# Performance work log

Measured on AMD Instinct MI355X. Metric: run time of the kernel, lower is better.

## Reference

```python
import jax, jax.numpy as jnp
import numpy as np

N = 200000          # nodes
E = 6400000         # edges (avg degree 32)
IN_C, HID, OUT_C = 128, 16, 2


def gcn_conv(x, W, b, src, dst, n):
    """PyG GCNConv: out = D^{-1/2} (A + I) D^{-1/2} (x W) + b."""
    h = x @ W  # transform first (in_channels >= out_channels): [n, d_out]
    loop = jnp.arange(n)
    s = jnp.concatenate([src, loop])  # add self-loops
    d = jnp.concatenate([dst, loop])
    ew = jnp.ones(s.shape[0], x.dtype)
    deg = jax.ops.segment_sum(ew, d, num_segments=n)  # in-degree incl. self-loop
    dinv = jnp.where(deg > 0, jax.lax.rsqrt(deg), jnp.zeros((), x.dtype))
    norm = dinv[s] * dinv[d]                          # [E+n]
    msg = h[s] * norm[:, None]                        # gather + scale
    out = jax.ops.segment_sum(msg, d, num_segments=n) # scatter-add
    return out + b


def setup_inputs() -> dict:
    key = jax.random.key(0)
    k1, k2, k3, k4 = jax.random.split(key, 4)
    x = jax.random.normal(k1, (N, IN_C), dtype=jnp.float32)
    edge_index = jax.random.randint(k2, (2, E), 0, N, dtype=jnp.int64)
    # Glorot-style init like PyG GCNConv
    W1 = jax.random.normal(k3, (IN_C, HID), dtype=jnp.float32) * (1.0 / np.sqrt(IN_C))
    b1 = jnp.zeros((HID,), jnp.float32)
    W2 = jax.random.normal(k4, (HID, OUT_C), dtype=jnp.float32) * (1.0 / np.sqrt(HID))
    b2 = jnp.zeros((OUT_C,), jnp.float32)
    return {"x": x, "edge_index": edge_index, "W1": W1, "b1": b1, "W2": W2, "b2": b2}


def reference(x, edge_index, W1, b1, W2, b2):
    src, dst = edge_index[0], edge_index[1]
    h = gcn_conv(x, W1, b1, src, dst, N)
    h = jax.nn.relu(h)
    return gcn_conv(h, W2, b2, src, dst, N)
```

## Files before the change

### kernel.cpp

```cpp
#include <hip/hip_runtime.h>
#include <hip/hip_fp16.h>

#define NN   200000
#define EE   6400000
#define INC  128
#define HIDC 16
#define OUTC 2

#define TN     256
#define TSHIFT 8
#define TMASK  (TN - 1)
#define NT     782
#define CHUNK  8192
#define NBE    782
#define SCAP   10240

__global__ __launch_bounds__(256) void k_hist(const int* __restrict__ dst,
                                              int* __restrict__ tile_counts) {
    __shared__ int h[NT];
    for (int t = threadIdx.x; t < NT; t += 256) h[t] = 0;
    __syncthreads();
    int base = blockIdx.x * CHUNK;
    if (base + CHUNK <= EE) {
        for (int i = threadIdx.x; i < CHUNK; i += 1024) {
            int d0 = dst[base + i];
            int d1 = dst[base + i + 256];
            int d2 = dst[base + i + 512];
            int d3 = dst[base + i + 768];
            atomicAdd(&h[d0 >> TSHIFT], 1);
            atomicAdd(&h[d1 >> TSHIFT], 1);
            atomicAdd(&h[d2 >> TSHIFT], 1);
            atomicAdd(&h[d3 >> TSHIFT], 1);
        }
    } else {
        for (int i = threadIdx.x; i < CHUNK; i += 256) {
            int e = base + i;
            if (e < EE) atomicAdd(&h[dst[e] >> TSHIFT], 1);
        }
    }
    __syncthreads();
    for (int t = threadIdx.x; t < NT; t += 256) {
        int c = h[t];
        if (c) atomicAdd(&tile_counts[t], c);
    }
}

__global__ __launch_bounds__(1024) void k_scan(const int* __restrict__ tile_counts,
                                               int* __restrict__ tile_base,
                                               int* __restrict__ gcur) {
    __shared__ int tmp[1024];
    int t = threadIdx.x;
    int v = (t < NT) ? tile_counts[t] : 0;
    tmp[t] = v;
    __syncthreads();
    for (int o = 1; o < 1024; o <<= 1) {
        int u = (t >= o) ? tmp[t - o] : 0;
        __syncthreads();
        tmp[t] += u;
        __syncthreads();
    }
    if (t < NT) {
        int ex = tmp[t] - v;
        tile_base[t] = ex;
        gcur[t] = ex;
    }
}

__global__ __launch_bounds__(256) void k_place(const int* __restrict__ src,
                                               const int* __restrict__ dst,
                                               int* __restrict__ gcur,
                                               int* __restrict__ brec) {
    __shared__ int h[NT];
    __shared__ int lbase[NT];
    __shared__ int gofs[NT];
    __shared__ int stmp[256];
    __shared__ int lrec[CHUNK];
    __shared__ unsigned short ltid[CHUNK];

    int tid = threadIdx.x;
    int base = blockIdx.x * CHUNK;
    int nrec = EE - base; if (nrec > CHUNK) nrec = CHUNK;
    bool full = (base + CHUNK <= EE);

    for (int t = tid; t < NT; t += 256) h[t] = 0;
    __syncthreads();
    if (full) {
        for (int i = tid; i < CHUNK; i += 1024) {
            int d0 = dst[base + i];
            int d1 = dst[base + i + 256];
            int d2 = dst[base + i + 512];
            int d3 = dst[base + i + 768];
            atomicAdd(&h[d0 >> TSHIFT], 1);
            atomicAdd(&h[d1 >> TSHIFT], 1);
            atomicAdd(&h[d2 >> TSHIFT], 1);
            atomicAdd(&h[d3 >> TSHIFT], 1);
        }
    } else {
        for (int i = tid; i < nrec; i += 256)
            atomicAdd(&h[dst[base + i] >> TSHIFT], 1);
    }
    __syncthreads();

    int t0 = tid * 4;
    int c0 = (t0 + 0 < NT) ? h[t0 + 0] : 0;
    int c1 = (t0 + 1 < NT) ? h[t0 + 1] : 0;
    int c2 = (t0 + 2 < NT) ? h[t0 + 2] : 0;
    int c3 = (t0 + 3 < NT) ? h[t0 + 3] : 0;
    int s = c0 + c1 + c2 + c3;
    stmp[tid] = s;
    __syncthreads();
    for (int o = 1; o < 256; o <<= 1) {
        int u = (tid >= o) ? stmp[tid - o] : 0;
        __syncthreads();
        stmp[tid] += u;
        __syncthreads();
    }
    int run = stmp[tid] - s;
    if (t0 + 0 < NT) { lbase[t0 + 0] = run; run += c0; }
    if (t0 + 1 < NT) { lbase[t0 + 1] = run; run += c1; }
    if (t0 + 2 < NT) { lbase[t0 + 2] = run; run += c2; }
    if (t0 + 3 < NT) { lbase[t0 + 3] = run; run += c3; }
    __syncthreads();

    for (int t = tid; t < NT; t += 256) {
        int c = h[t];
        int gb = c ? atomicAdd(&gcur[t], c) : 0;
        gofs[t] = gb - lbase[t];
    }
    __syncthreads();

    if (full) {
        for (int i = tid; i < CHUNK; i += 1024) {
            int e = base + i;
            int d0 = dst[e], d1 = dst[e + 256], d2 = dst[e + 512], d3 = dst[e + 768];
            int s0 = src[e], s1 = src[e + 256], s2 = src[e + 512], s3 = src[e + 768];
            int t0_ = d0 >> TSHIFT, t1_ = d1 >> TSHIFT;
            int t2_ = d2 >> TSHIFT, t3_ = d3 >> TSHIFT;
            int p0 = atomicAdd(&lbase[t0_], 1);
            int p1 = atomicAdd(&lbase[t1_], 1);
            int p2 = atomicAdd(&lbase[t2_], 1);
            int p3 = atomicAdd(&lbase[t3_], 1);
            lrec[p0] = (s0 << 8) | (d0 & TMASK); ltid[p0] = (unsigned short)t0_;
            lrec[p1] = (s1 << 8) | (d1 & TMASK); ltid[p1] = (unsigned short)t1_;
            lrec[p2] = (s2 << 8) | (d2 & TMASK); ltid[p2] = (unsigned short)t2_;
            lrec[p3] = (s3 << 8) | (d3 & TMASK); ltid[p3] = (unsigned short)t3_;
        }
    } else {
        for (int i = tid; i < nrec; i += 256) {
            int e = base + i;
            int d = dst[e], ss = src[e];
            int tt = d >> TSHIFT;
            int p = atomicAdd(&lbase[tt], 1);
            lrec[p] = (ss << 8) | (d & TMASK); ltid[p] = (unsigned short)tt;
        }
    }
    __syncthreads();

    for (int i = tid; i < nrec; i += 256) {
        int r = lrec[i];
        int tt = ltid[i];
        brec[gofs[tt] + i] = r;
    }
}

__global__ __launch_bounds__(256) void k_sortt(int* __restrict__ brec,
                                               const int* __restrict__ tile_base,
                                               const int* __restrict__ tile_counts,
                                               int* __restrict__ nstart,
                                               int* __restrict__ ndeg) {
    __shared__ int rec[SCAP];
    __shared__ int hist[TN];
    __shared__ int scn[TN];
    __shared__ int cur[TN];
    int t = blockIdx.x;
    int s0 = tile_base[t];
    int cnt = tile_counts[t];
    if (cnt > SCAP) cnt = SCAP;
    if (threadIdx.x < TN) hist[threadIdx.x] = 0;
    __syncthreads();
    for (int i = threadIdx.x; i < cnt; i += 256) {
        int r = brec[s0 + i];
        rec[i] = r;
        atomicAdd(&hist[r & TMASK], 1);
    }
    __syncthreads();
    if (threadIdx.x < TN) scn[threadIdx.x] = hist[threadIdx.x];
    __syncthreads();
    for (int o = 1; o < TN; o <<= 1) {
        int u = (threadIdx.x >= o && threadIdx.x < TN) ? scn[threadIdx.x - o] : 0;
        __syncthreads();
        if (threadIdx.x < TN) scn[threadIdx.x] += u;
        __syncthreads();
    }
    if (threadIdx.x < TN) {
        int ex = scn[threadIdx.x] - hist[threadIdx.x];
        cur[threadIdx.x] = ex;
        int node = t * TN + threadIdx.x;
        if (node < NN) {
            nstart[node] = s0 + ex;
            ndeg[node] = hist[threadIdx.x];
        }
    }
    __syncthreads();
    for (int i = threadIdx.x; i < cnt; i += 256) {
        int r = rec[i];
        int pos = atomicAdd(&cur[r & TMASK], 1);
        brec[s0 + pos] = r >> 8;
    }
}

__global__ __launch_bounds__(256) void k_xw(const float* __restrict__ x,
                                            const float* __restrict__ W1,
                                            const int* __restrict__ ndeg,
                                            __half2* __restrict__ g1) {
    __shared__ float Ws[INC * HIDC];
    for (int j = threadIdx.x; j < INC * HIDC; j += 256) Ws[j] = W1[j];
    __syncthreads();
    int n = blockIdx.x * 256 + threadIdx.x;
    if (n >= NN) return;
    const float4* xr = (const float4*)(x + (size_t)n * INC);
    float acc[HIDC];
#pragma unroll
    for (int c = 0; c < HIDC; ++c) acc[c] = 0.f;
    for (int k4 = 0; k4 < INC / 4; ++k4) {
        float4 xv = xr[k4];
        const float* w0 = &Ws[(k4 * 4) * HIDC];
        float xs[4] = {xv.x, xv.y, xv.z, xv.w};
#pragma unroll
        for (int j = 0; j < 4; ++j) {
#pragma unroll
            for (int c = 0; c < HIDC; ++c) acc[c] += xs[j] * w0[j * HIDC + c];
        }
    }
    float dn = rsqrtf((float)(ndeg[n] + 1));
    union { __half2 h[8]; float4 f[2]; } u;
#pragma unroll
    for (int q = 0; q < 8; ++q)
        u.h[q] = __floats2half2_rn(dn * acc[2 * q], dn * acc[2 * q + 1]);
    float4* gp = (float4*)(g1 + (size_t)n * 8);
    gp[0] = u.f[0];
    gp[1] = u.f[1];
}

__global__ __launch_bounds__(256) void k_agg1n(const int* __restrict__ csr,
                                               const int* __restrict__ nstart,
                                               const int* __restrict__ ndeg,
                                               const __half2* __restrict__ g1,
                                               const float* __restrict__ b1,
                                               const float* __restrict__ W2,
                                               float* __restrict__ g2) {
    int lane = threadIdx.x & 7;
    int n = (blockIdx.x * 256 + threadIdx.x) >> 3;
    if (n >= NN) return;
    int rs = nstart[n];
    int deg = ndeg[n];
    int re = rs + deg;
    float dn = rsqrtf((float)(deg + 1));
    float2 s = __half22float2(g1[(size_t)n * 8 + lane]);
    float ax = s.x, ay = s.y;
    int i = rs;
    for (; i + 4 <= re; i += 4) {
        int s0 = csr[i], s1 = csr[i + 1], s2 = csr[i + 2], s3 = csr[i + 3];
        float2 f0 = __half22float2(g1[(size_t)s0 * 8 + lane]);
        float2 f1 = __half22float2(g1[(size_t)s1 * 8 + lane]);
        float2 f2 = __half22float2(g1[(size_t)s2 * 8 + lane]);
        float2 f3 = __half22float2(g1[(size_t)s3 * 8 + lane]);
        ax += f0.x + f1.x + f2.x + f3.x;
        ay += f0.y + f1.y + f2.y + f3.y;
    }
    for (; i < re; ++i) {
        float2 f = __half22float2(g1[(size_t)csr[i] * 8 + lane]);
        ax += f.x; ay += f.y;
    }
    float h0 = fmaxf(fmaf(dn, ax, b1[2 * lane]), 0.f);
    float h1 = fmaxf(fmaf(dn, ay, b1[2 * lane + 1]), 0.f);
    float p0 = h0 * W2[(2 * lane) * OUTC + 0] + h1 * W2[(2 * lane + 1) * OUTC + 0];
    float p1 = h0 * W2[(2 * lane) * OUTC + 1] + h1 * W2[(2 * lane + 1) * OUTC + 1];
#pragma unroll
    for (int o = 4; o; o >>= 1) {
        p0 += __shfl_xor(p0, o, 8);
        p1 += __shfl_xor(p1, o, 8);
    }
    if (lane == 0) {
        float2 v; v.x = dn * p0; v.y = dn * p1;
        ((float2*)g2)[n] = v;
    }
}

__global__ __launch_bounds__(256) void k_agg2n(const int* __restrict__ csr,
                                               const int* __restrict__ nstart,
                                               const int* __restrict__ ndeg,
                                               const float* __restrict__ g2,
                                               const float* __restrict__ b2,
                                               float* __restrict__ out) {
    int lane = threadIdx.x & 7;
    int n = (blockIdx.x * 256 + threadIdx.x) >> 3;
    if (n >= NN) return;
    int rs = nstart[n];
    int deg = ndeg[n];
    int re = rs + deg;
    float dn = rsqrtf((float)(deg + 1));
    float ax = 0.f, ay = 0.f;
    for (int i = rs + lane; i < re; i += 8) {
        float2 v = ((const float2*)g2)[csr[i]];
        ax += v.x; ay += v.y;
    }
#pragma unroll
    for (int o = 4; o; o >>= 1) {
        ax += __shfl_xor(ax, o, 8);
        ay += __shfl_xor(ay, o, 8);
    }
    if (lane == 0) {
        float2 g = ((const float2*)g2)[n];
        float2 o2;
        o2.x = fmaf(dn, ax + g.x, b2[0]);
        o2.y = fmaf(dn, ay + g.y, b2[1]);
        ((float2*)out)[n] = o2;
    }
}


__global__ void k_deg_f(const int* __restrict__ dst, int* __restrict__ deg) {
    int i = blockIdx.x * blockDim.x + threadIdx.x;
    if (i < EE) atomicAdd(&deg[dst[i]], 1);
}
__global__ void k_dinv_f(const int* __restrict__ deg, float* __restrict__ dinv) {
    int n = blockIdx.x * blockDim.x + threadIdx.x;
    if (n < NN) dinv[n] = rsqrtf((float)(deg[n] + 1));
}
__global__ void k_xw_f(const float* __restrict__ x, const float* __restrict__ W1,
                       const float* __restrict__ dinv, float* __restrict__ g1) {
    __shared__ float Ws[INC * HIDC];
    for (int j = threadIdx.x; j < INC * HIDC; j += 256) Ws[j] = W1[j];
    __syncthreads();
    int n = blockIdx.x * 256 + threadIdx.x;
    if (n >= NN) return;
    const float4* xr = (const float4*)(x + (size_t)n * INC);
    float acc[HIDC];
#pragma unroll
    for (int c = 0; c < HIDC; ++c) acc[c] = 0.f;
    for (int k4 = 0; k4 < INC / 4; ++k4) {
        float4 xv = xr[k4];
        const float* w0 = &Ws[(k4 * 4) * HIDC];
        float xs[4] = {xv.x, xv.y, xv.z, xv.w};
#pragma unroll
        for (int j = 0; j < 4; ++j)
#pragma unroll
            for (int c = 0; c < HIDC; ++c) acc[c] += xs[j] * w0[j * HIDC + c];
    }
    float dn = dinv[n];
#pragma unroll
    for (int c = 0; c < HIDC; ++c) g1[(size_t)n * HIDC + c] = dn * acc[c];
}
__global__ void k_scatter1_f(const int* __restrict__ src, const int* __restrict__ dst,
                             const float* __restrict__ g1, float* __restrict__ acc1) {
    int i = blockIdx.x * blockDim.x + threadIdx.x;
    if (i >= EE * 4) return;
    int e = i >> 2, q = i & 3;
    float4 v = ((const float4*)g1)[src[e] * 4 + q];
    float* p = acc1 + (size_t)dst[e] * HIDC + q * 4;
    unsafeAtomicAdd(p + 0, v.x); unsafeAtomicAdd(p + 1, v.y);
    unsafeAtomicAdd(p + 2, v.z); unsafeAtomicAdd(p + 3, v.w);
}
__global__ void k_l2_f(const float* __restrict__ g1, const float* __restrict__ acc1,
                       const float* __restrict__ dinv, const float* __restrict__ b1,
                       const float* __restrict__ W2, float* __restrict__ g2) {
    int n = blockIdx.x * blockDim.x + threadIdx.x;
    if (n >= NN) return;
    float dn = dinv[n];
    float h[HIDC];
#pragma unroll
    for (int c = 0; c < HIDC; ++c)
        h[c] = fmaxf(dn * (acc1[(size_t)n * HIDC + c] + g1[(size_t)n * HIDC + c]) + b1[c], 0.f);
    float o0 = 0.f, o1 = 0.f;
#pragma unroll
    for (int c = 0; c < HIDC; ++c) { o0 += h[c] * W2[c * 2]; o1 += h[c] * W2[c * 2 + 1]; }
    g2[(size_t)n * 2] = dn * o0; g2[(size_t)n * 2 + 1] = dn * o1;
}
__global__ void k_scatter2_f(const int* __restrict__ src, const int* __restrict__ dst,
                             const float* __restrict__ g2, float* __restrict__ acc2) {
    int e = blockIdx.x * blockDim.x + threadIdx.x;
    if (e >= EE) return;
    float2 v = ((const float2*)g2)[src[e]];
    unsafeAtomicAdd(&acc2[(size_t)dst[e] * 2], v.x);
    unsafeAtomicAdd(&acc2[(size_t)dst[e] * 2 + 1], v.y);
}
__global__ void k_final_f(const float* __restrict__ g2, const float* __restrict__ acc2,
                          const float* __restrict__ dinv, const float* __restrict__ b2,
                          float* __restrict__ out) {
    int n = blockIdx.x * blockDim.x + threadIdx.x;
    if (n >= NN) return;
    float dn = dinv[n];
    float2 a = ((const float2*)acc2)[n];
    float2 g = ((const float2*)g2)[n];
    float2 o;
    o.x = dn * (a.x + g.x) + b2[0];
    o.y = dn * (a.y + g.y) + b2[1];
    ((float2*)out)[n] = o;
}


extern "C" void kernel_launch(void* const* d_in, const int* in_sizes, int n_in,
                              void* d_out, int out_size, void* d_ws, size_t ws_size,
                              hipStream_t stream) {
    const float* x  = (const float*)d_in[0];
    const int*   ei = (const int*)d_in[1];
    const float* W1 = (const float*)d_in[2];
    const float* b1 = (const float*)d_in[3];
    const float* W2 = (const float*)d_in[4];
    const float* b2 = (const float*)d_in[5];
    float* out = (float*)d_out;

    const int* src = ei;
    const int* dst = ei + EE;
    const int B = 256;

    size_t need = ((size_t)3 * NT + EE + (size_t)(NN + 1) + (size_t)NN +
                   (size_t)8 * NN + (size_t)2 * NN) * 4;
    if (ws_size >= need) {
        int* ws          = (int*)d_ws;
        int* tile_counts = ws;
        int* tile_base   = ws + NT;
        int* gcur        = ws + 2 * NT;
        int* brec        = ws + 3 * NT;
        int* nstart      = brec + EE;
        int* ndeg        = nstart + NN + 1;
        __half2* g1      = (__half2*)(ndeg + NN);
        float* g2        = (float*)((int*)(ndeg + NN) + (size_t)8 * NN);

        hipMemsetAsync(tile_counts, 0, (size_t)NT * 4, stream);

        k_hist  <<<NBE, 256, 0, stream>>>(dst, tile_counts);
        k_scan  <<<1, 1024, 0, stream>>>(tile_counts, tile_base, gcur);
        k_place <<<NBE, 256, 0, stream>>>(src, dst, gcur, brec);
        k_sortt <<<NT, 256, 0, stream>>>(brec, tile_base, tile_counts, nstart, ndeg);
        k_xw    <<<(NN + 255) / 256, 256, 0, stream>>>(x, W1, ndeg, g1);
        k_agg1n <<<(NN * 8 + 255) / 256, 256, 0, stream>>>(brec, nstart, ndeg, g1, b1, W2, g2);
        k_agg2n <<<(NN * 8 + 255) / 256, 256, 0, stream>>>(brec, nstart, ndeg, g2, b2, out);
        return;
    }

    char* wsb = (char*)d_ws;
    int*   deg  = (int*)wsb;
    float* acc1 = (float*)(wsb + (size_t)NN * 4);
    float* acc2 = (float*)(wsb + (size_t)17 * NN * 4);
    float* dinv = (float*)(wsb + (size_t)19 * NN * 4);
    float* g1   = (float*)(wsb + (size_t)20 * NN * 4);
    float* g2   = (float*)(wsb + (size_t)36 * NN * 4);

    hipMemsetAsync(d_ws, 0, (size_t)19 * NN * 4, stream);

    int gN = (NN + B - 1) / B, gE = (EE + B - 1) / B, gE4 = (EE * 4 + B - 1) / B;
    k_deg_f     <<<gE, B, 0, stream>>>(dst, deg);
    k_dinv_f    <<<gN, B, 0, stream>>>(deg, dinv);
    k_xw_f      <<<gN, B, 0, stream>>>(x, W1, dinv, g1);
    k_scatter1_f<<<gE4, B, 0, stream>>>(src, dst, g1, acc1);
    k_l2_f      <<<gN, B, 0, stream>>>(g1, acc1, dinv, b1, W2, g2);
    k_scatter2_f<<<gE, B, 0, stream>>>(src, dst, g2, acc2);
    k_final_f   <<<gN, B, 0, stream>>>(g2, acc2, dinv, b2, out);
}
```

Before: 451.0 us.

## Split layer-1 feature table into two halves and aggregate in two passes

The fp16 hidden-feature table is split into two 8-channel halves of 3.2 MB each, written separately by the XW kernel. Layer-1 aggregation runs as two passes, each gathering from one half with 4 lanes per node, so the random-access working set is smaller and more likely to stay in cache. In exchange the CSR index array and node metadata are read twice, and a partial-result buffer is written and then read back between the passes.

Measured after the change: 474.8 us. +5.3%, slower.

```diff
diff --git a/kernel.cpp b/kernel.cpp
--- a/kernel.cpp
+++ b/kernel.cpp
@@ -212,7 +212,8 @@
 __global__ __launch_bounds__(256) void k_xw(const float* __restrict__ x,
                                             const float* __restrict__ W1,
                                             const int* __restrict__ ndeg,
-                                            __half2* __restrict__ g1) {
+                                            __half2* __restrict__ g1a,
+                                            __half2* __restrict__ g1b) {
     __shared__ float Ws[INC * HIDC];
     for (int j = threadIdx.x; j < INC * HIDC; j += 256) Ws[j] = W1[j];
     __syncthreads();
@@ -237,53 +238,58 @@
 #pragma unroll
     for (int q = 0; q < 8; ++q)
         u.h[q] = __floats2half2_rn(dn * acc[2 * q], dn * acc[2 * q + 1]);
-    float4* gp = (float4*)(g1 + (size_t)n * 8);
-    gp[0] = u.f[0];
-    gp[1] = u.f[1];
-}
-
-__global__ __launch_bounds__(256) void k_agg1n(const int* __restrict__ csr,
+    ((float4*)(g1a + (size_t)n * 4))[0] = u.f[0];
+    ((float4*)(g1b + (size_t)n * 4))[0] = u.f[1];
+}
+
+__global__ __launch_bounds__(256) void k_agg1h(const int* __restrict__ csr,
                                                const int* __restrict__ nstart,
                                                const int* __restrict__ ndeg,
-                                               const __half2* __restrict__ g1,
+                                               const __half2* __restrict__ tab,
                                                const float* __restrict__ b1,
                                                const float* __restrict__ W2,
-                                               float* __restrict__ g2) {
-    int lane = threadIdx.x & 7;
-    int n = (blockIdx.x * 256 + threadIdx.x) >> 3;
+                                               float* __restrict__ pacc,
+                                               float* __restrict__ g2,
+                                               int cofs, int phase) {
+    int lane = threadIdx.x & 3;
+    int n = (blockIdx.x * 256 + threadIdx.x) >> 2;
     if (n >= NN) return;
     int rs = nstart[n];
     int deg = ndeg[n];
     int re = rs + deg;
     float dn = rsqrtf((float)(deg + 1));
-    float2 s = __half22float2(g1[(size_t)n * 8 + lane]);
-    float ax = s.x, ay = s.y;
+    float2 sl = __half22float2(tab[(size_t)n * 4 + lane]);
+    float ax = sl.x, ay = sl.y;
     int i = rs;
     for (; i + 4 <= re; i += 4) {
         int s0 = csr[i], s1 = csr[i + 1], s2 = csr[i + 2], s3 = csr[i + 3];
-        float2 f0 = __half22float2(g1[(size_t)s0 * 8 + lane]);
-        float2 f1 = __half22float2(g1[(size_t)s1 * 8 + lane]);
-        float2 f2 = __half22float2(g1[(size_t)s2 * 8 + lane]);
-        float2 f3 = __half22float2(g1[(size_t)s3 * 8 + lane]);
+        float2 f0 = __half22float2(tab[(size_t)s0 * 4 + lane]);
+        float2 f1 = __half22float2(tab[(size_t)s1 * 4 + lane]);
+        float2 f2 = __half22float2(tab[(size_t)s2 * 4 + lane]);
+        float2 f3 = __half22float2(tab[(size_t)s3 * 4 + lane]);
         ax += f0.x + f1.x + f2.x + f3.x;
         ay += f0.y + f1.y + f2.y + f3.y;
     }
     for (; i < re; ++i) {
-        float2 f = __half22float2(g1[(size_t)csr[i] * 8 + lane]);
+        float2 f = __half22float2(tab[(size_t)csr[i] * 4 + lane]);
         ax += f.x; ay += f.y;
     }
-    float h0 = fmaxf(fmaf(dn, ax, b1[2 * lane]), 0.f);
-    float h1 = fmaxf(fmaf(dn, ay, b1[2 * lane + 1]), 0.f);
-    float p0 = h0 * W2[(2 * lane) * OUTC + 0] + h1 * W2[(2 * lane + 1) * OUTC + 0];
-    float p1 = h0 * W2[(2 * lane) * OUTC + 1] + h1 * W2[(2 * lane + 1) * OUTC + 1];
-#pragma unroll
-    for (int o = 4; o; o >>= 1) {
-        p0 += __shfl_xor(p0, o, 8);
-        p1 += __shfl_xor(p1, o, 8);
-    }
+    int c0 = cofs + 2 * lane;
+    float h0 = fmaxf(fmaf(dn, ax, b1[c0]), 0.f);
+    float h1 = fmaxf(fmaf(dn, ay, b1[c0 + 1]), 0.f);
+    float p0 = h0 * W2[c0 * OUTC + 0] + h1 * W2[(c0 + 1) * OUTC + 0];
+    float p1 = h0 * W2[c0 * OUTC + 1] + h1 * W2[(c0 + 1) * OUTC + 1];
+    p0 += __shfl_xor(p0, 1, 4); p0 += __shfl_xor(p0, 2, 4);
+    p1 += __shfl_xor(p1, 1, 4); p1 += __shfl_xor(p1, 2, 4);
     if (lane == 0) {
-        float2 v; v.x = dn * p0; v.y = dn * p1;
-        ((float2*)g2)[n] = v;
+        if (phase == 0) {
+            float2 v; v.x = p0; v.y = p1;
+            ((float2*)pacc)[n] = v;
+        } else {
+            float2 pa = ((const float2*)pacc)[n];
+            float2 v; v.x = dn * (p0 + pa.x); v.y = dn * (p1 + pa.y);
+            ((float2*)g2)[n] = v;
+        }
     }
 }
 
@@ -416,7 +422,7 @@
     const int B = 256;
 
     size_t need = ((size_t)3 * NT + EE + (size_t)(NN + 1) + (size_t)NN +
-                   (size_t)8 * NN + (size_t)2 * NN) * 4;
+                   (size_t)4 * NN + (size_t)4 * NN + (size_t)2 * NN + (size_t)2 * NN) * 4;
     if (ws_size >= need) {
         int* ws          = (int*)d_ws;
         int* tile_counts = ws;
@@ -425,8 +431,10 @@
         int* brec        = ws + 3 * NT;
         int* nstart      = brec + EE;
         int* ndeg        = nstart + NN + 1;
-        __half2* g1      = (__half2*)(ndeg + NN);
-        float* g2        = (float*)((int*)(ndeg + NN) + (size_t)8 * NN);
+        __half2* g1a     = (__half2*)(ndeg + NN);
+        __half2* g1b     = g1a + (size_t)4 * NN;
+        float* pacc      = (float*)(g1b + (size_t)4 * NN);
+        float* g2        = pacc + (size_t)2 * NN;
 
         hipMemsetAsync(tile_counts, 0, (size_t)NT * 4, stream);
 
@@ -434,8 +442,9 @@
         k_scan  <<<1, 1024, 0, stream>>>(tile_counts, tile_base, gcur);
         k_place <<<NBE, 256, 0, stream>>>(src, dst, gcur, brec);
         k_sortt <<<NT, 256, 0, stream>>>(brec, tile_base, tile_counts, nstart, ndeg);
-        k_xw    <<<(NN + 255) / 256, 256, 0, stream>>>(x, W1, ndeg, g1);
-        k_agg1n <<<(NN * 8 + 255) / 256, 256, 0, stream>>>(brec, nstart, ndeg, g1, b1, W2, g2);
+        k_xw    <<<(NN + 255) / 256, 256, 0, stream>>>(x, W1, ndeg, g1a, g1b);
+        k_agg1h <<<(NN * 4 + 255) / 256, 256, 0, stream>>>(brec, nstart, ndeg, g1a, b1, W2, pacc, g2, 0, 0);
+        k_agg1h <<<(NN * 4 + 255) / 256, 256, 0, stream>>>(brec, nstart, ndeg, g1b, b1, W2, pacc, g2, 8, 1);
         k_agg2n <<<(NN * 8 + 255) / 256, 256, 0, stream>>>(brec, nstart, ndeg, g2, b2, out);
         return;
     }
```
